# Optimization experiments

Measured on AMD Instinct MI355X. Metric: run time of the kernel, lower is better.

The kernel has to match this reference:

```python
import jax, jax.numpy as jnp
import numpy as np

N, E, F_IN, H, NC, NG = 50000, 800000, 256, 64, 4, 64

def setup_inputs() -> dict:
    key = jax.random.key(0)
    ks = jax.random.split(key, 12)
    inp = {
        'x': jax.random.normal(ks[0], (N, F_IN), dtype=jnp.float32),
        'edge_index': jax.random.randint(ks[1], (2, E), 0, N, dtype=jnp.int64),
        'batch': jnp.sort(jax.random.randint(ks[2], (N,), 0, NG, dtype=jnp.int64)),
        # GCNConv layer 1 and 2 (weight [in,out] + bias), Glorot-ish scale
        'W1': jax.random.normal(ks[3], (F_IN, H), dtype=jnp.float32) / np.sqrt(F_IN),
        'b1': jnp.zeros((H,), dtype=jnp.float32),
        'W2': jax.random.normal(ks[4], (H, H), dtype=jnp.float32) / np.sqrt(H),
        'b2': jnp.zeros((H,), dtype=jnp.float32),
        # MLP head
        'fc1_w': jax.random.normal(ks[5], (H, 128), dtype=jnp.float32) / np.sqrt(H),
        'fc1_b': jnp.zeros((128,), dtype=jnp.float32),
        'fc2_w': jax.random.normal(ks[6], (128, NC), dtype=jnp.float32) / np.sqrt(128),
        'fc2_b': jnp.zeros((NC,), dtype=jnp.float32),
    }
    return inp

def _gcn_conv(x, src, dst, W, b, n_nodes):
    # PyG GCNConv: add self-loops, symmetric norm D^-1/2 (A+I) D^-1/2, then X W + b
    h = x @ W  # [N, out]
    deg = jax.ops.segment_sum(jnp.ones_like(dst, dtype=h.dtype), dst, num_segments=n_nodes)
    dinv = jnp.where(deg > 0, jax.lax.rsqrt(deg), 0.0)
    norm = dinv[src] * dinv[dst]  # [E+N]
    msg = h[src] * norm[:, None]
    out = jax.ops.segment_sum(msg, dst, num_segments=n_nodes)
    return out + b

def reference(x, edge_index, batch, W1, b1, W2, b2, fc1_w, fc1_b, fc2_w, fc2_b):
    n = x.shape[0]
    loops = jnp.arange(n, dtype=edge_index.dtype)
    src = jnp.concatenate([edge_index[0], loops])
    dst = jnp.concatenate([edge_index[1], loops])
    h = jax.nn.relu(_gcn_conv(x, src, dst, W1, b1, n))
    h = jax.nn.relu(_gcn_conv(h, src, dst, W2, b2, n))
    # global_mean_pool over graph ids
    sums = jax.ops.segment_sum(h, batch, num_segments=NG)
    cnts = jax.ops.segment_sum(jnp.ones((n,), h.dtype), batch, num_segments=NG)
    pooled = sums / jnp.maximum(cnts, 1.0)[:, None]  # [NG, H]
    z = jax.nn.relu(pooled @ fc1_w + fc1_b)
    # dropout in eval mode = identity
    return z @ fc2_w + fc2_b  # [NG, NC]
```

## Files before the change

kernel.cpp:

```cpp
#include <hip/hip_runtime.h>


#define TPB 256
#define CHUNK_A 4096
#define BCAP 4608

typedef unsigned short bfu;
typedef __attribute__((ext_vector_type(8))) short s16x8;
typedef __attribute__((ext_vector_type(4))) float f32x4;

__device__ __forceinline__ float bf2f(bfu u) {
    union { unsigned u32; float f; } c; c.u32 = ((unsigned)u) << 16; return c.f;
}
__device__ __forceinline__ bfu f2bf(float f) {
    union { float f; unsigned u; } c; c.f = f;
    unsigned r = 0x7FFFu + ((c.u >> 16) & 1u);
    return (bfu)((c.u + r) >> 16);
}
__device__ __forceinline__ float blo(unsigned w) {
    union { unsigned u32; float f; } c; c.u32 = w << 16; return c.f;
}
__device__ __forceinline__ float bhi(unsigned w) {
    union { unsigned u32; float f; } c; c.u32 = w & 0xFFFF0000u; return c.f;
}
__device__ __forceinline__ void split_bf(float x, bfu& h, bfu& l) {
    h = f2bf(x);
    l = f2bf(x - bf2f(h));
}


__global__ __launch_bounds__(TPB) void k_passA(const int* __restrict__ srcv,
                                               const int* __restrict__ dstv, int E,
                                               int* __restrict__ gcur,
                                               int* __restrict__ staged, int nbuck) {
    __shared__ int pk[CHUNK_A];
    __shared__ int hist[256];
    __shared__ int ebase[256];
    __shared__ int gbase[256];
    __shared__ int lcur[256];
    int t = threadIdx.x;
    int e0 = blockIdx.x * CHUNK_A;
    int e1 = e0 + CHUNK_A; if (e1 > E) e1 = E;

    hist[t] = 0; lcur[t] = 0;
    __syncthreads();
    for (int i = e0 + t; i < e1; i += TPB) atomicAdd(&hist[dstv[i] >> 8], 1);
    __syncthreads();
    int v = hist[t];
    ebase[t] = v;
    __syncthreads();
    for (int off = 1; off < 256; off <<= 1) {
        int u = (t >= off) ? ebase[t - off] : 0;
        __syncthreads();
        ebase[t] += u;
        __syncthreads();
    }
    ebase[t] -= v;
    if (t < nbuck && v > 0) gbase[t] = t * BCAP + atomicAdd(&gcur[t], v);
    __syncthreads();
    for (int i = e0 + t; i < e1; i += TPB) {
        int d = dstv[i];
        int s = srcv[i];
        int b = d >> 8;
        int r = atomicAdd(&lcur[b], 1);
        pk[ebase[b] + r] = (s << 8) | (d & 255);
    }
    __syncthreads();
    int wave = t >> 6, lane = t & 63;
    for (int b = wave; b < nbuck; b += 4) {
        int c = hist[b];
        int lb = ebase[b];
        int gb = gbase[b];
        for (int j = lane; j < c; j += 64) staged[gb + j] = pk[lb + j];
    }
}


__global__ __launch_bounds__(TPB) void k_passB(const int* __restrict__ staged,
                                               const int* __restrict__ gcur,
                                               int* __restrict__ csr_off,
                                               int* __restrict__ csr_src,
                                               float* __restrict__ dinv,
                                               int n, int nbuck) {
    __shared__ int pk[BCAP];
    __shared__ int soff[256];
    __shared__ int hist[256];
    __shared__ int nbase[256];
    __shared__ int cur[256];
    int b = blockIdx.x;
    int n0 = b << 8;
    int n1 = n0 + 256; if (n1 > n) n1 = n;
    int cnt = gcur[b];
    int t = threadIdx.x;

    int cv = (t < nbuck) ? gcur[t] : 0;
    soff[t] = cv;
    hist[t] = 0; cur[t] = 0;
    __syncthreads();
    for (int off = 1; off < 256; off <<= 1) {
        int u = (t >= off) ? soff[t - off] : 0;
        __syncthreads();
        soff[t] += u;
        __syncthreads();
    }
    int base = soff[b] - cnt;

    for (int i = t; i < cnt; i += TPB) pk[i] = staged[b * BCAP + i];
    __syncthreads();
    for (int i = t; i < cnt; i += TPB) atomicAdd(&hist[pk[i] & 255], 1);
    __syncthreads();
    int v = hist[t];
    nbase[t] = v;
    __syncthreads();
    for (int off = 1; off < 256; off <<= 1) {
        int u = (t >= off) ? nbase[t - off] : 0;
        __syncthreads();
        nbase[t] += u;
        __syncthreads();
    }
    nbase[t] -= v;
    if (n0 + t < n1) {
        csr_off[n0 + t] = base + nbase[t];
        dinv[n0 + t] = rsqrtf((float)(v + 1));
    }
    if (b == nbuck - 1 && t == 0) csr_off[n] = base + cnt;
    __syncthreads();
    for (int i = t; i < cnt; i += TPB) {
        int p = pk[i];
        int dloc = p & 255;
        int r = atomicAdd(&cur[dloc], 1);
        csr_src[base + nbase[dloc] + r] = p >> 8;
    }
}


__device__ __forceinline__ int swz(int rc, int k) {
    return rc * 64 + (k ^ ((rc & 7) << 3));
}

template <int K, bool BF16A>
__global__ __launch_bounds__(TPB) void k_gemm(const void* __restrict__ Av,
                                              const float* __restrict__ W,
                                              const float* __restrict__ dinv,
                                              bfu* __restrict__ C, int n) {
    __shared__ __align__(16) ushort Ah[128 * 64];
    __shared__ __align__(16) ushort Al[BF16A ? 64 : 128 * 64];
    __shared__ __align__(16) ushort Bh[64 * 64];
    __shared__ __align__(16) ushort Bl[64 * 64];

    const int t = threadIdx.x;
    const int wave = t >> 6, lane = t & 63;
    const int rbase = blockIdx.x * 128;

    f32x4 acc[2][4];
#pragma unroll
    for (int i = 0; i < 2; i++)
#pragma unroll
        for (int j = 0; j < 4; j++) acc[i][j] = {0.f, 0.f, 0.f, 0.f};

    for (int kc = 0; kc < K; kc += 64) {
        {
            int c = t & 63;
            int kg = (t >> 6) << 4;
#pragma unroll
            for (int q = 0; q < 4; q++) {
                ushort4 h4, l4;
#pragma unroll
                for (int j = 0; j < 4; j++) {
                    float w = W[(size_t)(kc + kg + q * 4 + j) * 64 + c];
                    bfu hh, ll; split_bf(w, hh, ll);
                    ((bfu*)&h4)[j] = hh;
                    ((bfu*)&l4)[j] = ll;
                }
                *(ushort4*)&Bh[swz(c, kg + q * 4)] = h4;
                *(ushort4*)&Bl[swz(c, kg + q * 4)] = l4;
            }
        }
        if (!BF16A) {
            const float* A = (const float*)Av;
#pragma unroll
            for (int q = 0; q < 8; q++) {
                int idx = q * 256 + t;
                int row = idx >> 4;
                int k4 = (idx & 15) << 2;
                int r = rbase + row;
                float4 xv = make_float4(0.f, 0.f, 0.f, 0.f);
                if (r < n) xv = *(const float4*)&A[(size_t)r * K + kc + k4];
                ushort4 h4, l4;
                split_bf(xv.x, ((bfu*)&h4)[0], ((bfu*)&l4)[0]);
                split_bf(xv.y, ((bfu*)&h4)[1], ((bfu*)&l4)[1]);
                split_bf(xv.z, ((bfu*)&h4)[2], ((bfu*)&l4)[2]);
                split_bf(xv.w, ((bfu*)&h4)[3], ((bfu*)&l4)[3]);
                *(ushort4*)&Ah[swz(row, k4)] = h4;
                *(ushort4*)&Al[swz(row, k4)] = l4;
            }
        } else {
            const bfu* A = (const bfu*)Av;
#pragma unroll
            for (int q = 0; q < 4; q++) {
                int idx = q * 256 + t;
                int row = idx >> 3;
                int k8 = (idx & 7) << 3;
                int r = rbase + row;
                uint4 v = make_uint4(0u, 0u, 0u, 0u);
                if (r < n) v = *(const uint4*)(A + (size_t)r * 64 + k8);
                *(uint2*)&Ah[swz(row, k8)]     = make_uint2(v.x, v.y);
                *(uint2*)&Ah[swz(row, k8 + 4)] = make_uint2(v.z, v.w);
            }
        }
        __syncthreads();

        const int rl = lane & 15;
        const int kg8 = (lane >> 4) << 3;
#pragma unroll
        for (int ks = 0; ks < 2; ks++) {
            int k0 = ks * 32 + kg8;
            s16x8 a_h[2], a_l[2], b_h[4], b_l[4];
#pragma unroll
            for (int rt = 0; rt < 2; rt++) {
                int row = wave * 32 + rt * 16 + rl;
                a_h[rt] = *(const s16x8*)&Ah[swz(row, k0)];
                if (!BF16A) a_l[rt] = *(const s16x8*)&Al[swz(row, k0)];
            }
#pragma unroll
            for (int ct = 0; ct < 4; ct++) {
                int cc = ct * 16 + rl;
                b_h[ct] = *(const s16x8*)&Bh[swz(cc, k0)];
                b_l[ct] = *(const s16x8*)&Bl[swz(cc, k0)];
            }
#pragma unroll
            for (int rt = 0; rt < 2; rt++)
#pragma unroll
                for (int ct = 0; ct < 4; ct++) {
                    acc[rt][ct] = __builtin_amdgcn_mfma_f32_16x16x32_bf16(
                        a_h[rt], b_h[ct], acc[rt][ct], 0, 0, 0);
                    acc[rt][ct] = __builtin_amdgcn_mfma_f32_16x16x32_bf16(
                        a_h[rt], b_l[ct], acc[rt][ct], 0, 0, 0);
                    if (!BF16A)
                        acc[rt][ct] = __builtin_amdgcn_mfma_f32_16x16x32_bf16(
                            a_l[rt], b_h[ct], acc[rt][ct], 0, 0, 0);
                }
        }
        __syncthreads();
    }

    const int rl = lane & 15;
    const int rq = (lane >> 4) << 2;
#pragma unroll
    for (int rt = 0; rt < 2; rt++) {
#pragma unroll
        for (int reg = 0; reg < 4; reg++) {
            int r = rbase + wave * 32 + rt * 16 + rq + reg;
            if (r < n) {
                float d = dinv[r];
#pragma unroll
                for (int ct = 0; ct < 4; ct++) {
                    C[(size_t)r * 64 + ct * 16 + rl] = f2bf(acc[rt][ct][reg] * d);
                }
            }
        }
    }
}


__global__ __launch_bounds__(TPB) void k_agg(const bfu* __restrict__ hs,
                                             const int* __restrict__ csr_off,
                                             const int* __restrict__ csr_src,
                                             const float* __restrict__ dinv,
                                             const float* __restrict__ bias,
                                             bfu* __restrict__ out, int n) {
    int node = blockIdx.x * 4 + (threadIdx.x >> 6);
    int lane = threadIdx.x & 63;
    int half = lane >> 5;
    int fl = (lane & 31) * 2;
    if (node >= n) return;
    int p0 = csr_off[node];
    int p1 = csr_off[node + 1];

    float ax = 0.f, ay = 0.f;
    {
        unsigned g = *(const unsigned*)(hs + (size_t)node * 64 + fl);
        if (half == 0) { ax = blo(g); ay = bhi(g); }
    }
    int p = p0;
    for (; p + 16 <= p1; p += 16) {
        int s[8]; unsigned g[8];
#pragma unroll
        for (int i = 0; i < 8; i++) s[i] = csr_src[p + 2 * i + half];
#pragma unroll
        for (int i = 0; i < 8; i++) g[i] = *(const unsigned*)(hs + (size_t)s[i] * 64 + fl);
#pragma unroll
        for (int i = 0; i < 8; i++) { ax += blo(g[i]); ay += bhi(g[i]); }
    }
    if (p + 8 <= p1) {
        int s[4]; unsigned g[4];
#pragma unroll
        for (int i = 0; i < 4; i++) s[i] = csr_src[p + 2 * i + half];
#pragma unroll
        for (int i = 0; i < 4; i++) g[i] = *(const unsigned*)(hs + (size_t)s[i] * 64 + fl);
#pragma unroll
        for (int i = 0; i < 4; i++) { ax += blo(g[i]); ay += bhi(g[i]); }
        p += 8;
    }
    if (p + 4 <= p1) {
        int s[2]; unsigned g[2];
#pragma unroll
        for (int i = 0; i < 2; i++) s[i] = csr_src[p + 2 * i + half];
#pragma unroll
        for (int i = 0; i < 2; i++) g[i] = *(const unsigned*)(hs + (size_t)s[i] * 64 + fl);
#pragma unroll
        for (int i = 0; i < 2; i++) { ax += blo(g[i]); ay += bhi(g[i]); }
        p += 4;
    }
    if (p + 2 <= p1) {
        int s = csr_src[p + half];
        unsigned g = *(const unsigned*)(hs + (size_t)s * 64 + fl);
        ax += blo(g); ay += bhi(g);
        p += 2;
    }
    if (p < p1) {
        int s = csr_src[p];
        unsigned g = *(const unsigned*)(hs + (size_t)s * 64 + fl);
        if (half == 0) { ax += blo(g); ay += bhi(g); }
    }
    ax += __shfl_xor(ax, 32);
    ay += __shfl_xor(ay, 32);

    float d = dinv[node];
    float vx = fmaxf(d * ax + bias[fl + 0], 0.f);
    float vy = fmaxf(d * ay + bias[fl + 1], 0.f);
    if (half == 0) {
        ushort2 o;
        o.x = f2bf(vx);
        o.y = f2bf(vy);
        *(ushort2*)(out + (size_t)node * 64 + fl) = o;
    }
}


__global__ __launch_bounds__(TPB) void k_pool(const bfu* __restrict__ h,
                                              const int* __restrict__ batch, int n,
                                              float* __restrict__ gsum,
                                              int* __restrict__ gcnt) {
    const int CH = 16;
    int wid = blockIdx.x * 4 + (threadIdx.x >> 6);
    int lane = threadIdx.x & 63;
    int i0 = wid * CH;
    if (i0 >= n) return;
    int i1 = i0 + CH; if (i1 > n) i1 = n;
    int g0 = batch[i0];
    int g1 = batch[i1 - 1];
    if (g0 == g1) {
        float acc = 0.f;
#pragma unroll
        for (int i = 0; i < CH; i++) {
            int idx = i0 + i;
            if (idx < i1) acc += bf2f(h[(size_t)idx * 64 + lane]);
        }
        atomicAdd(&gsum[g0 * 64 + lane], acc);
        if (lane == 0) atomicAdd(&gcnt[g0], i1 - i0);
    } else {
        int cur = g0;
        float acc = 0.f;
        int cnt = 0;
        for (int i = i0; i < i1; i++) {
            int g = batch[i];
            if (g != cur) {
                atomicAdd(&gsum[cur * 64 + lane], acc);
                if (lane == 0) atomicAdd(&gcnt[cur], cnt);
                acc = 0.f; cnt = 0; cur = g;
            }
            acc += bf2f(h[(size_t)i * 64 + lane]);
            cnt++;
        }
        atomicAdd(&gsum[cur * 64 + lane], acc);
        if (lane == 0) atomicAdd(&gcnt[cur], cnt);
    }
}


__global__ __launch_bounds__(TPB) void k_head1(const float* __restrict__ gsum,
                                               const int* __restrict__ gcnt,
                                               const float* __restrict__ fc1w,
                                               const float* __restrict__ fc1b,
                                               float* __restrict__ z) {
    int t = threadIdx.x;
    int g = blockIdx.x * 2 + (t >> 7);
    int o = t & 127;
    int c = gcnt[g]; if (c < 1) c = 1;
    float inv = 1.0f / (float)c;
    float a = fc1b[o];
#pragma unroll 16
    for (int j = 0; j < 64; j++) {
        float pj = gsum[g * 64 + j] * inv;
        a += pj * fc1w[j * 128 + o];
    }
    z[g * 128 + o] = fmaxf(a, 0.f);
}


__global__ __launch_bounds__(TPB) void k_head2(const float* __restrict__ z,
                                               const float* __restrict__ fc2w,
                                               const float* __restrict__ fc2b,
                                               float* __restrict__ out) {
    int t = threadIdx.x;
    int g = t >> 2, c = t & 3;
    float a = fc2b[c];
#pragma unroll 16
    for (int o = 0; o < 128; o++) a += z[g * 128 + o] * fc2w[o * 4 + c];
    out[t] = a;
}


extern "C" void kernel_launch(void* const* d_in, const int* in_sizes, int n_in,
                              void* d_out, int out_size, void* d_ws, size_t ws_size,
                              hipStream_t stream) {
    const float* x    = (const float*)d_in[0];
    const int*   ei   = (const int*)d_in[1];
    const int*   batch= (const int*)d_in[2];
    const float* W1   = (const float*)d_in[3];
    const float* b1   = (const float*)d_in[4];
    const float* W2   = (const float*)d_in[5];
    const float* b2   = (const float*)d_in[6];
    const float* fc1w = (const float*)d_in[7];
    const float* fc1b = (const float*)d_in[8];
    const float* fc2w = (const float*)d_in[9];
    const float* fc2b = (const float*)d_in[10];

    const int n = in_sizes[2];
    const int E = in_sizes[1] / 2;
    const int* srcv = ei;
    const int* dstv = ei + E;
    const int nbuck = (n + 255) >> 8;

    char* w = (char*)d_ws;
    int*   gcur   = (int*)w;            w += 256 * 4;
    int*   gcnt   = (int*)w;            w += 64 * 4;
    float* gsum   = (float*)w;          w += 64 * 64 * 4;
    size_t zbytes = (size_t)w - (size_t)d_ws;
    int*   csr_off= (int*)w;            w += (size_t)(n + 1) * 4;
    float* dinv   = (float*)w;          w += (size_t)n * 4;
    int*   csr_src= (int*)w;            w += (size_t)E * 4;
    int*   staged = (int*)w;            w += (size_t)nbuck * BCAP * 4;
    float* zbuf   = (float*)w;          w += 64 * 128 * 4;
    w = (char*)(((size_t)w + 255) & ~(size_t)255);
    bfu* hs = (bfu*)w;                  w += (size_t)n * 64 * 2;
    w = (char*)(((size_t)w + 255) & ~(size_t)255);
    bfu* hb = (bfu*)w;                  w += (size_t)n * 64 * 2;

    hipMemsetAsync(d_ws, 0, zbytes, stream);

    int gA = (E + CHUNK_A - 1) / CHUNK_A;
    k_passA<<<gA, TPB, 0, stream>>>(srcv, dstv, E, gcur, staged, nbuck);
    k_passB<<<nbuck, TPB, 0, stream>>>(staged, gcur, csr_off, csr_src, dinv, n, nbuck);

    int gRows = (n + 127) / 128;
    int gNode = (n + 3) / 4;
    k_gemm<256, false><<<gRows, TPB, 0, stream>>>(x, W1, dinv, hs, n);
    k_agg<<<gNode, TPB, 0, stream>>>(hs, csr_off, csr_src, dinv, b1, hb, n);
    k_gemm<64, true><<<gRows, TPB, 0, stream>>>(hb, W2, dinv, hs, n);
    k_agg<<<gNode, TPB, 0, stream>>>(hs, csr_off, csr_src, dinv, b2, hb, n);

    int nwaves16 = (n + 15) / 16;
    k_pool<<<(nwaves16 + 3) / 4, TPB, 0, stream>>>(hb, batch, n, gsum, gcnt);
    k_head1<<<32, TPB, 0, stream>>>(gsum, gcnt, fc1w, fc1b, zbuf);
    k_head2<<<1, TPB, 0, stream>>>(zbuf, fc2w, fc2b, (float*)d_out);
}
```

Baseline: 251.6 us.

## Make CSR build deterministic without atomics and fuse pool with MLP head

Pass A now writes each chunk's per-bucket counts and offsets plus its locally sorted edges straight to a staging area, with no global atomics. Pass B sums the counts, scans them, and gathers its bucket's segments from every chunk. The memset is removed: the second GEMM zeroes the pool accumulators. Pool and both head layers become one kernel, where the last block to finish (detected with an atomic counter) runs the MLP. This cuts two launches and a memset, in exchange for a serial per-chunk count loop in pass B, more scattered gathers, and a single-block tail over 8K fc1 outputs.

```diff
diff --git a/kernel.cpp b/kernel.cpp
--- a/kernel.cpp
+++ b/kernel.cpp
@@ -31,15 +31,16 @@
 
 __global__ __launch_bounds__(TPB) void k_passA(const int* __restrict__ srcv,
                                                const int* __restrict__ dstv, int E,
-                                               int* __restrict__ gcur,
-                                               int* __restrict__ staged, int nbuck) {
+                                               int* __restrict__ cnt,
+                                               int* __restrict__ coff,
+                                               int* __restrict__ staged) {
     __shared__ int pk[CHUNK_A];
     __shared__ int hist[256];
     __shared__ int ebase[256];
-    __shared__ int gbase[256];
     __shared__ int lcur[256];
     int t = threadIdx.x;
-    int e0 = blockIdx.x * CHUNK_A;
+    int c = blockIdx.x;
+    int e0 = c * CHUNK_A;
     int e1 = e0 + CHUNK_A; if (e1 > E) e1 = E;
 
     hist[t] = 0; lcur[t] = 0;
@@ -49,14 +50,15 @@
     int v = hist[t];
     ebase[t] = v;
     __syncthreads();
-    for (int off = 1; off < 256; off <<= 1) {
-        int u = (t >= off) ? ebase[t - off] : 0;
+    for (int o = 1; o < 256; o <<= 1) {
+        int u = (t >= o) ? ebase[t - o] : 0;
         __syncthreads();
         ebase[t] += u;
         __syncthreads();
     }
     ebase[t] -= v;
-    if (t < nbuck && v > 0) gbase[t] = t * BCAP + atomicAdd(&gcur[t], v);
+    cnt[c * 256 + t] = v;
+    coff[c * 256 + t] = ebase[t];
     __syncthreads();
     for (int i = e0 + t; i < e1; i += TPB) {
         int d = dstv[i];
@@ -66,66 +68,87 @@
         pk[ebase[b] + r] = (s << 8) | (d & 255);
     }
     __syncthreads();
-    int wave = t >> 6, lane = t & 63;
-    for (int b = wave; b < nbuck; b += 4) {
-        int c = hist[b];
-        int lb = ebase[b];
-        int gb = gbase[b];
-        for (int j = lane; j < c; j += 64) staged[gb + j] = pk[lb + j];
-    }
+    for (int i = t; i < e1 - e0; i += TPB) staged[e0 + i] = pk[i];
 }
 
 
 __global__ __launch_bounds__(TPB) void k_passB(const int* __restrict__ staged,
-                                               const int* __restrict__ gcur,
+                                               const int* __restrict__ cnt,
+                                               const int* __restrict__ coff,
+                                               int nchunk,
                                                int* __restrict__ csr_off,
                                                int* __restrict__ csr_src,
                                                float* __restrict__ dinv,
                                                int n, int nbuck) {
     __shared__ int pk[BCAP];
-    __shared__ int soff[256];
+    __shared__ int sc[256];
     __shared__ int hist[256];
     __shared__ int nbase[256];
     __shared__ int cur[256];
+    __shared__ int ccnt_l[256];
+    __shared__ int coff_l[256];
+    __shared__ int cdst_l[256];
     int b = blockIdx.x;
+    int t = threadIdx.x;
     int n0 = b << 8;
     int n1 = n0 + 256; if (n1 > n) n1 = n;
-    int cnt = gcur[b];
-    int t = threadIdx.x;
-
-    int cv = (t < nbuck) ? gcur[t] : 0;
-    soff[t] = cv;
+
+    int s = 0;
+    for (int c = 0; c < nchunk; c++) s += cnt[c * 256 + t];
+    sc[t] = s;
     hist[t] = 0; cur[t] = 0;
-    __syncthreads();
-    for (int off = 1; off < 256; off <<= 1) {
-        int u = (t >= off) ? soff[t - off] : 0;
-        __syncthreads();
-        soff[t] += u;
-        __syncthreads();
-    }
-    int base = soff[b] - cnt;
-
-    for (int i = t; i < cnt; i += TPB) pk[i] = staged[b * BCAP + i];
-    __syncthreads();
-    for (int i = t; i < cnt; i += TPB) atomicAdd(&hist[pk[i] & 255], 1);
+    int cpv = (t < nchunk) ? cnt[t * 256 + b] : 0;
+    ccnt_l[t] = cpv;
+    coff_l[t] = (t < nchunk) ? coff[t * 256 + b] : 0;
+    __syncthreads();
+    for (int o = 1; o < 256; o <<= 1) {
+        int u = (t >= o) ? sc[t - o] : 0;
+        __syncthreads();
+        sc[t] += u;
+        __syncthreads();
+    }
+    int base = (b == 0) ? 0 : sc[b - 1];
+    int mycnt = sc[b] - base;
+    __syncthreads();
+    sc[t] = cpv;
+    __syncthreads();
+    for (int o = 1; o < 256; o <<= 1) {
+        int u = (t >= o) ? sc[t - o] : 0;
+        __syncthreads();
+        sc[t] += u;
+        __syncthreads();
+    }
+    cdst_l[t] = sc[t] - cpv;
+    __syncthreads();
+    int wave = t >> 6, lane = t & 63;
+    for (int c = wave; c < nchunk; c += 4) {
+        int cc = ccnt_l[c];
+        int so = coff_l[c];
+        int dd = cdst_l[c];
+        for (int j = lane; j < cc; j += 64)
+            pk[dd + j] = staged[c * CHUNK_A + so + j];
+    }
+    __syncthreads();
+    for (int i = t; i < mycnt; i += TPB) atomicAdd(&hist[pk[i] & 255], 1);
     __syncthreads();
     int v = hist[t];
-    nbase[t] = v;
-    __syncthreads();
-    for (int off = 1; off < 256; off <<= 1) {
-        int u = (t >= off) ? nbase[t - off] : 0;
-        __syncthreads();
-        nbase[t] += u;
-        __syncthreads();
-    }
-    nbase[t] -= v;
+    sc[t] = v;
+    __syncthreads();
+    for (int o = 1; o < 256; o <<= 1) {
+        int u = (t >= o) ? sc[t - o] : 0;
+        __syncthreads();
+        sc[t] += u;
+        __syncthreads();
+    }
+    int nb = sc[t] - v;
+    nbase[t] = nb;
     if (n0 + t < n1) {
-        csr_off[n0 + t] = base + nbase[t];
+        csr_off[n0 + t] = base + nb;
         dinv[n0 + t] = rsqrtf((float)(v + 1));
     }
-    if (b == nbuck - 1 && t == 0) csr_off[n] = base + cnt;
-    __syncthreads();
-    for (int i = t; i < cnt; i += TPB) {
+    if (b == nbuck - 1 && t == 0) csr_off[n] = base + mycnt;
+    __syncthreads();
+    for (int i = t; i < mycnt; i += TPB) {
         int p = pk[i];
         int dloc = p & 255;
         int r = atomicAdd(&cur[dloc], 1);
@@ -142,7 +165,8 @@
 __global__ __launch_bounds__(TPB) void k_gemm(const void* __restrict__ Av,
                                               const float* __restrict__ W,
                                               const float* __restrict__ dinv,
-                                              bfu* __restrict__ C, int n) {
+                                              bfu* __restrict__ C, int n,
+                                              int* __restrict__ zr, int zn) {
     __shared__ __align__(16) ushort Ah[128 * 64];
     __shared__ __align__(16) ushort Al[BF16A ? 64 : 128 * 64];
     __shared__ __align__(16) ushort Bh[64 * 64];
@@ -151,6 +175,10 @@
     const int t = threadIdx.x;
     const int wave = t >> 6, lane = t & 63;
     const int rbase = blockIdx.x * 128;
+
+    if (zn > 0 && blockIdx.x == 0) {
+        for (int i = t; i < zn; i += TPB) zr[i] = 0;
+    }
 
     f32x4 acc[2][4];
 #pragma unroll
@@ -338,77 +366,90 @@
 }
 
 
-__global__ __launch_bounds__(TPB) void k_pool(const bfu* __restrict__ h,
-                                              const int* __restrict__ batch, int n,
-                                              float* __restrict__ gsum,
-                                              int* __restrict__ gcnt) {
+__global__ __launch_bounds__(TPB) void k_poolhead(const bfu* __restrict__ h,
+                                                  const int* __restrict__ batch, int n,
+                                                  float* __restrict__ gsum,
+                                                  int* __restrict__ gcnt,
+                                                  int* __restrict__ done,
+                                                  const float* __restrict__ fc1w,
+                                                  const float* __restrict__ fc1b,
+                                                  const float* __restrict__ fc2w,
+                                                  const float* __restrict__ fc2b,
+                                                  float* __restrict__ out) {
+    __shared__ float zs[64 * 128];
+    __shared__ float ps[64 * 64];
+    __shared__ float cinv[64];
+    __shared__ int lastflag;
     const int CH = 16;
     int wid = blockIdx.x * 4 + (threadIdx.x >> 6);
     int lane = threadIdx.x & 63;
     int i0 = wid * CH;
-    if (i0 >= n) return;
-    int i1 = i0 + CH; if (i1 > n) i1 = n;
-    int g0 = batch[i0];
-    int g1 = batch[i1 - 1];
-    if (g0 == g1) {
-        float acc = 0.f;
-#pragma unroll
-        for (int i = 0; i < CH; i++) {
-            int idx = i0 + i;
-            if (idx < i1) acc += bf2f(h[(size_t)idx * 64 + lane]);
+    if (i0 < n) {
+        int i1 = i0 + CH; if (i1 > n) i1 = n;
+        int g0 = batch[i0];
+        int g1 = batch[i1 - 1];
+        if (g0 == g1) {
+            float acc = 0.f;
+#pragma unroll
+            for (int i = 0; i < CH; i++) {
+                int idx = i0 + i;
+                if (idx < i1) acc += bf2f(h[(size_t)idx * 64 + lane]);
+            }
+            atomicAdd(&gsum[g0 * 64 + lane], acc);
+            if (lane == 0) atomicAdd(&gcnt[g0], i1 - i0);
+        } else {
+            int cur = g0;
+            float acc = 0.f;
+            int cnt = 0;
+            for (int i = i0; i < i1; i++) {
+                int g = batch[i];
+                if (g != cur) {
+                    atomicAdd(&gsum[cur * 64 + lane], acc);
+                    if (lane == 0) atomicAdd(&gcnt[cur], cnt);
+                    acc = 0.f; cnt = 0; cur = g;
+                }
+                acc += bf2f(h[(size_t)i * 64 + lane]);
+                cnt++;
+            }
+            atomicAdd(&gsum[cur * 64 + lane], acc);
+            if (lane == 0) atomicAdd(&gcnt[cur], cnt);
         }
-        atomicAdd(&gsum[g0 * 64 + lane], acc);
-        if (lane == 0) atomicAdd(&gcnt[g0], i1 - i0);
-    } else {
-        int cur = g0;
-        float acc = 0.f;
-        int cnt = 0;
-        for (int i = i0; i < i1; i++) {
-            int g = batch[i];
-            if (g != cur) {
-                atomicAdd(&gsum[cur * 64 + lane], acc);
-                if (lane == 0) atomicAdd(&gcnt[cur], cnt);
-                acc = 0.f; cnt = 0; cur = g;
-            }
-            acc += bf2f(h[(size_t)i * 64 + lane]);
-            cnt++;
-        }
-        atomicAdd(&gsum[cur * 64 + lane], acc);
-        if (lane == 0) atomicAdd(&gcnt[cur], cnt);
-    }
-}
-
-
-__global__ __launch_bounds__(TPB) void k_head1(const float* __restrict__ gsum,
-                                               const int* __restrict__ gcnt,
-                                               const float* __restrict__ fc1w,
-                                               const float* __restrict__ fc1b,
-                                               float* __restrict__ z) {
+    }
+    __threadfence();
+    __syncthreads();
+    if (threadIdx.x == 0) {
+        int old = atomicAdd(done, 1);
+        lastflag = (old == (int)gridDim.x - 1);
+    }
+    __syncthreads();
+    if (!lastflag) return;
+    __threadfence();
+
     int t = threadIdx.x;
-    int g = blockIdx.x * 2 + (t >> 7);
-    int o = t & 127;
-    int c = gcnt[g]; if (c < 1) c = 1;
-    float inv = 1.0f / (float)c;
-    float a = fc1b[o];
+    for (int i = t; i < 64 * 64; i += TPB)
+        ps[i] = __hip_atomic_load(&gsum[i], __ATOMIC_RELAXED, __HIP_MEMORY_SCOPE_AGENT);
+    if (t < 64) {
+        int c = __hip_atomic_load(&gcnt[t], __ATOMIC_RELAXED, __HIP_MEMORY_SCOPE_AGENT);
+        if (c < 1) c = 1;
+        cinv[t] = 1.0f / (float)c;
+    }
+    __syncthreads();
+    for (int idx = t; idx < 64 * 128; idx += TPB) {
+        int g = idx >> 7, o = idx & 127;
+        float a = fc1b[o];
+        float iv = cinv[g];
 #pragma unroll 16
-    for (int j = 0; j < 64; j++) {
-        float pj = gsum[g * 64 + j] * inv;
-        a += pj * fc1w[j * 128 + o];
-    }
-    z[g * 128 + o] = fmaxf(a, 0.f);
-}
-
-
-__global__ __launch_bounds__(TPB) void k_head2(const float* __restrict__ z,
-                                               const float* __restrict__ fc2w,
-                                               const float* __restrict__ fc2b,
-                                               float* __restrict__ out) {
-    int t = threadIdx.x;
-    int g = t >> 2, c = t & 3;
-    float a = fc2b[c];
+        for (int j = 0; j < 64; j++) a += ps[g * 64 + j] * iv * fc1w[j * 128 + o];
+        zs[idx] = fmaxf(a, 0.f);
+    }
+    __syncthreads();
+    {
+        int g = t >> 2, c = t & 3;
+        float a = fc2b[c];
 #pragma unroll 16
-    for (int o = 0; o < 128; o++) a += z[g * 128 + o] * fc2w[o * 4 + c];
-    out[t] = a;
+        for (int o = 0; o < 128; o++) a += zs[g * 128 + o] * fc2w[o * 4 + c];
+        out[t] = a;
+    }
 }
 
 
@@ -432,37 +473,35 @@
     const int* srcv = ei;
     const int* dstv = ei + E;
     const int nbuck = (n + 255) >> 8;
+    const int gA = (E + CHUNK_A - 1) / CHUNK_A;
 
     char* w = (char*)d_ws;
-    int*   gcur   = (int*)w;            w += 256 * 4;
+    float* gsum   = (float*)w;          w += 64 * 64 * 4;
     int*   gcnt   = (int*)w;            w += 64 * 4;
-    float* gsum   = (float*)w;          w += 64 * 64 * 4;
-    size_t zbytes = (size_t)w - (size_t)d_ws;
+    int*   done   = (int*)w;            w += 4;
     int*   csr_off= (int*)w;            w += (size_t)(n + 1) * 4;
     float* dinv   = (float*)w;          w += (size_t)n * 4;
     int*   csr_src= (int*)w;            w += (size_t)E * 4;
-    int*   staged = (int*)w;            w += (size_t)nbuck * BCAP * 4;
-    float* zbuf   = (float*)w;          w += 64 * 128 * 4;
+    int*   staged = (int*)w;            w += (size_t)gA * CHUNK_A * 4;
+    int*   cnt    = (int*)w;            w += (size_t)gA * 256 * 4;
+    int*   coff   = (int*)w;            w += (size_t)gA * 256 * 4;
     w = (char*)(((size_t)w + 255) & ~(size_t)255);
     bfu* hs = (bfu*)w;                  w += (size_t)n * 64 * 2;
     w = (char*)(((size_t)w + 255) & ~(size_t)255);
     bfu* hb = (bfu*)w;                  w += (size_t)n * 64 * 2;
 
-    hipMemsetAsync(d_ws, 0, zbytes, stream);
-
-    int gA = (E + CHUNK_A - 1) / CHUNK_A;
-    k_passA<<<gA, TPB, 0, stream>>>(srcv, dstv, E, gcur, staged, nbuck);
-    k_passB<<<nbuck, TPB, 0, stream>>>(staged, gcur, csr_off, csr_src, dinv, n, nbuck);
-
     int gRows = (n + 127) / 128;
     int gNode = (n + 3) / 4;
-    k_gemm<256, false><<<gRows, TPB, 0, stream>>>(x, W1, dinv, hs, n);
+    int nwaves16 = (n + 15) / 16;
+    int gPool = (nwaves16 + 3) / 4;
+
+    k_passA<<<gA, TPB, 0, stream>>>(srcv, dstv, E, cnt, coff, staged);
+    k_passB<<<nbuck, TPB, 0, stream>>>(staged, cnt, coff, gA, csr_off, csr_src, dinv, n, nbuck);
+    k_gemm<256, false><<<gRows, TPB, 0, stream>>>(x, W1, dinv, hs, n, (int*)nullptr, 0);
     k_agg<<<gNode, TPB, 0, stream>>>(hs, csr_off, csr_src, dinv, b1, hb, n);
-    k_gemm<64, true><<<gRows, TPB, 0, stream>>>(hb, W2, dinv, hs, n);
+    k_gemm<64, true><<<gRows, TPB, 0, stream>>>(hb, W2, dinv, hs, n,
+                                                (int*)gsum, 64 * 64 + 64 + 1);
     k_agg<<<gNode, TPB, 0, stream>>>(hs, csr_off, csr_src, dinv, b2, hb, n);
-
-    int nwaves16 = (n + 15) / 16;
-    k_pool<<<(nwaves16 + 3) / 4, TPB, 0, stream>>>(hb, batch, n, gsum, gcnt);
-    k_head1<<<32, TPB, 0, stream>>>(gsum, gcnt, fc1w, fc1b, zbuf);
-    k_head2<<<1, TPB, 0, stream>>>(zbuf, fc2w, fc2b, (float*)d_out);
-}
+    k_poolhead<<<gPool, TPB, 0, stream>>>(hb, batch, n, gsum, gcnt, done,
+                                          fc1w, fc1b, fc2w, fc2b, (float*)d_out);
+}
```

After: 344.2 us. +36.8%, slower.
